# Optimization experiments

Hardware: AMD Instinct MI355X
Metric: run time of the kernel (lower is better)

## Reference

```python
import jax, jax.numpy as jnp
import numpy as np

B = 512
NV = 6890   # SMPL vertices
NJ = 24     # SMPL joints
NB = 10     # shape betas
NP = 207    # pose blend coeffs = 23*9
# canonical SMPL kinematic tree: parent of joints 1..23
PARENT = np.array([0, 0, 0, 1, 2, 3, 4, 5, 6, 7, 8, 9, 9, 9, 12, 13, 14, 16, 17, 18, 19, 20, 21], dtype=np.int64)


def quat2mat(quat):
    # quat: [N,4] (w,x,y,z) -> [N,3,3]
    q = quat / jnp.linalg.norm(quat, axis=1, keepdims=True)
    w, x, y, z = q[:, 0], q[:, 1], q[:, 2], q[:, 3]
    w2, x2, y2, z2 = w * w, x * x, y * y, z * z
    wx, wy, wz = w * x, w * y, w * z
    xy, xz, yz = x * y, x * z, y * z
    rot = jnp.stack([
        w2 + x2 - y2 - z2, 2 * xy - 2 * wz, 2 * wy + 2 * xz,
        2 * wz + 2 * xy, w2 - x2 + y2 - z2, 2 * yz - 2 * wx,
        2 * xz - 2 * wy, 2 * wx + 2 * yz, w2 - x2 - y2 + z2], axis=1)
    return rot.reshape(-1, 3, 3)


def rodrigues(theta):
    # theta: [N,3] axis-angle -> [N,3,3]
    angle = jnp.linalg.norm(theta + 1e-8, axis=1, keepdims=True)
    normalized = theta / angle
    half = angle * 0.5
    quat = jnp.concatenate([jnp.cos(half), jnp.sin(half) * normalized], axis=1)
    return quat2mat(quat)


def setup_inputs() -> dict:
    key = jax.random.key(0)
    ks = jax.random.split(key, 8)
    pose = jax.random.normal(ks[0], (B, NJ * 3), dtype=jnp.float32) * 0.2
    beta = jax.random.normal(ks[1], (B, NB), dtype=jnp.float32)
    v_template = jax.random.normal(ks[2], (NV, 3), dtype=jnp.float32)
    shapedirs = jax.random.normal(ks[3], (NV, 3, NB), dtype=jnp.float32) * 0.01
    posedirs = jax.random.normal(ks[4], (NV, 3, NP), dtype=jnp.float32) * 0.01
    Jr = jax.random.uniform(ks[5], (NJ, NV), dtype=jnp.float32)
    J_regressor = Jr / jnp.sum(Jr, axis=1, keepdims=True)
    W = jax.random.uniform(ks[6], (NV, NJ), dtype=jnp.float32)
    weights = W / jnp.sum(W, axis=1, keepdims=True)
    return {"pose": pose, "beta": beta, "v_template": v_template,
            "shapedirs": shapedirs, "posedirs": posedirs,
            "J_regressor": J_regressor, "weights": weights,
            "parent": PARENT}


def reference(pose, beta, v_template, shapedirs, posedirs, J_regressor, weights, parent):
    dt = pose.dtype
    bsz = pose.shape[0]
    # shape blend: v_shaped [B,V,3]
    v_shaped = jnp.einsum('vdk,bk->bvd', shapedirs, beta) + v_template[None]
    J = jnp.einsum('jv,bvd->bjd', J_regressor, v_shaped)  # [B,24,3]
    # per-joint rotations from axis-angle
    R = rodrigues(pose.reshape(-1, 3)).reshape(bsz, NJ, 3, 3)
    # pose blend
    I3 = jnp.eye(3, dtype=dt)
    lrotmin = (R[:, 1:] - I3).reshape(bsz, NP)
    v_posed = v_shaped + jnp.einsum('vdp,bp->bvd', posedirs, lrotmin)
    # relative joint locations
    J_rel = jnp.concatenate([J[:, :1], J[:, 1:] - J[:, parent]], axis=1)
    # local 4x4 transforms G_local [B,24,4,4]
    bottom = jnp.broadcast_to(jnp.array([0., 0., 0., 1.], dtype=dt).reshape(1, 1, 1, 4), (bsz, NJ, 1, 4))
    G_local = jnp.concatenate([jnp.concatenate([R, J_rel[..., None]], axis=-1), bottom], axis=2)
    # forward kinematics along the tree (24 fixed steps)
    Gs = [G_local[:, 0]]
    for i in range(1, NJ):
        Gs.append(jnp.matmul(Gs[int(parent[i - 1])], G_local[:, i]))
    G = jnp.stack(Gs, axis=1)  # [B,24,4,4]
    # subtract rest-pose joint contribution from translation column
    J_h = jnp.concatenate([J, jnp.zeros((bsz, NJ, 1), dtype=dt)], axis=-1)  # [B,24,4]
    t_corr = jnp.einsum('bjmn,bjn->bjm', G, J_h)
    G = G.at[..., 3].add(-t_corr)
    # linear blend skinning
    T = jnp.einsum('vj,bjmn->bvmn', weights, G)  # [B,V,4,4]
    v_h = jnp.concatenate([v_posed, jnp.ones((bsz, NV, 1), dtype=dt)], axis=-1)
    v = jnp.einsum('bvmn,bvn->bvm', T, v_h)[..., :3]  # [B,V,3]
    return v
```

## Files before the change

kernel.cpp:

```cpp
#include <hip/hip_runtime.h>
#include <hip/hip_bf16.h>
#include <math.h>

#define NVERT 6890
#define NJN   24
#define NBETA 10
#define NPOSE 207
#define NBATCH 512
#define KDIM  224
#define NCOL  20670
#define NPAD  20736

typedef __attribute__((ext_vector_type(8))) short bh8;
typedef __attribute__((ext_vector_type(4))) float f4;

__device__ const int c_parent[23] = {0,0,0,1,2,3,4,5,6,7,8,9,9,9,12,13,14,16,17,18,19,20,21};


__global__ void k_prep(const float* __restrict__ pd, const float* __restrict__ sh,
                       const float* __restrict__ wts,
                       __hip_bfloat16* __restrict__ Bt, float* __restrict__ wT) {
    const int btTotal = NPAD * KDIM;
    const int wtTotal = NJN * NVERT;
    const int total = btTotal + wtTotal;
    for (int idx = blockIdx.x * blockDim.x + threadIdx.x; idx < total;
         idx += gridDim.x * blockDim.x) {
        if (idx < btTotal) {
            int col = idx / KDIM;
            int k = idx - col * KDIM;
            float val = 0.0f;
            if (col < NCOL) {
                int v = col / 3, d = col - v * 3;
                if (k < NPOSE)      val = pd[v * 621 + d * 207 + k];
                else if (k < 217)   val = sh[v * 30 + d * 10 + (k - 207)];
            }
            Bt[idx] = __float2bfloat16(val);
        } else {
            int r = idx - btTotal;
            int j = r / NVERT, v = r - j * NVERT;
            wT[j * 6912 + v] = wts[v * NJN + j];
        }
    }
}

__global__ void k_jreg(const float* __restrict__ Jr, const float* __restrict__ vt,
                       const float* __restrict__ sh, float* __restrict__ jb) {
    const int jd = blockIdx.x;
    const int j = jd / 3, d = jd % 3;
    float acc[11];
#pragma unroll
    for (int k = 0; k < 11; k++) acc[k] = 0.0f;
    for (int v = threadIdx.x; v < NVERT; v += 256) {
        float r = Jr[j * NVERT + v];
        acc[0] += r * vt[v * 3 + d];
        const float* sp = sh + v * 30 + d * 10;
#pragma unroll
        for (int k = 0; k < 10; k++) acc[1 + k] += r * sp[k];
    }
#pragma unroll
    for (int k = 0; k < 11; k++) {
#pragma unroll
        for (int off = 32; off > 0; off >>= 1)
            acc[k] += __shfl_down(acc[k], off);
    }
    __shared__ float red[4][11];
    const int lane = threadIdx.x & 63, wid = threadIdx.x >> 6;
    if (lane == 0) {
#pragma unroll
        for (int k = 0; k < 11; k++) red[wid][k] = acc[k];
    }
    __syncthreads();
    if (threadIdx.x == 0) {
#pragma unroll
        for (int k = 0; k < 11; k++) {
            float s = red[0][k] + red[1][k] + red[2][k] + red[3][k];
            if (k == 0) jb[jd] = s;
            else jb[72 + jd * 10 + (k - 1)] = s;
        }
    }
}

__global__ void k_pose(const float* __restrict__ pose, const float* __restrict__ beta,
                       const float* __restrict__ jb, __hip_bfloat16* __restrict__ A,
                       float* __restrict__ g3) {
    const int b = blockIdx.x, t = threadIdx.x;
    __shared__ float sR[24][9], sJ[24][3], sGl[24][12], sG[24][12];
    if (t < 24) {
        const float* th = pose + b * 72 + t * 3;
        float tx = th[0], ty = th[1], tz = th[2];
        float ax = tx + 1e-8f, ay = ty + 1e-8f, az = tz + 1e-8f;
        float ang = sqrtf(ax * ax + ay * ay + az * az);
        float inv = 1.0f / ang;
        float nx = tx * inv, ny = ty * inv, nz = tz * inv;
        float sw, cw;
        sincosf(0.5f * ang, &sw, &cw);
        float qw = cw, qx = sw * nx, qy = sw * ny, qz = sw * nz;
        float qn = 1.0f / sqrtf(qw * qw + qx * qx + qy * qy + qz * qz);
        qw *= qn; qx *= qn; qy *= qn; qz *= qn;
        float w2 = qw * qw, x2 = qx * qx, y2 = qy * qy, z2 = qz * qz;
        float wx = qw * qx, wy = qw * qy, wz = qw * qz;
        float xy = qx * qy, xz = qx * qz, yz = qy * qz;
        float R[9];
        R[0] = w2 + x2 - y2 - z2; R[1] = 2.f * (xy - wz); R[2] = 2.f * (wy + xz);
        R[3] = 2.f * (wz + xy);   R[4] = w2 - x2 + y2 - z2; R[5] = 2.f * (yz - wx);
        R[6] = 2.f * (xz - wy);   R[7] = 2.f * (wx + yz);   R[8] = w2 - x2 - y2 + z2;
#pragma unroll
        for (int k = 0; k < 9; k++) sR[t][k] = R[k];
        if (t >= 1) {
            __hip_bfloat16* ap = A + b * KDIM + (t - 1) * 9;
#pragma unroll
            for (int k = 0; k < 9; k++)
                ap[k] = __float2bfloat16(R[k] - ((k == 0 || k == 4 || k == 8) ? 1.f : 0.f));
        }
    }
    if (t < NBETA) A[b * KDIM + 207 + t] = __float2bfloat16(beta[b * NBETA + t]);
    if (t < 7)     A[b * KDIM + 217 + t] = __float2bfloat16(0.0f);
    if (t < 72) {
        const int j = t / 3;
        float Jv = jb[t];
        const float* c = jb + 72 + t * 10;
        const float* be = beta + b * NBETA;
#pragma unroll
        for (int k = 0; k < 10; k++) Jv += c[k] * be[k];
        sJ[j][t - j * 3] = Jv;
    }
    __syncthreads();
    if (t < 24) {
#pragma unroll
        for (int r = 0; r < 3; r++) {
            sGl[t][r * 4 + 0] = sR[t][r * 3 + 0];
            sGl[t][r * 4 + 1] = sR[t][r * 3 + 1];
            sGl[t][r * 4 + 2] = sR[t][r * 3 + 2];
            float jr = sJ[t][r];
            if (t > 0) jr -= sJ[c_parent[t - 1]][r];
            sGl[t][r * 4 + 3] = jr;
        }
    }
    __syncthreads();
    if (t < 12) sG[0][t] = sGl[0][t];
    __syncthreads();
    for (int i = 1; i < 24; i++) {
        if (t < 12) {
            const int m = t >> 2, n = t & 3;
            const int p = c_parent[i - 1];
            float val = sG[p][m * 4 + 0] * sGl[i][0 + n]
                      + sG[p][m * 4 + 1] * sGl[i][4 + n]
                      + sG[p][m * 4 + 2] * sGl[i][8 + n];
            if (n == 3) val += sG[p][m * 4 + 3];
            sG[i][t] = val;
        }
        __syncthreads();
    }
    if (t < 24) {
        float jx = sJ[t][0], jy = sJ[t][1], jz = sJ[t][2];
        float* gp = g3 + b * 288 + t * 12;
#pragma unroll
        for (int m = 0; m < 3; m++) {
            float g0 = sG[t][m * 4 + 0], g1 = sG[t][m * 4 + 1];
            float g2 = sG[t][m * 4 + 2], g3v = sG[t][m * 4 + 3];
            float tc = g0 * jx + g1 * jy + g2 * jz;
            gp[m * 4 + 0] = g0; gp[m * 4 + 1] = g1;
            gp[m * 4 + 2] = g2; gp[m * 4 + 3] = g3v - tc;
        }
    }
}

__global__ __launch_bounds__(256) void k_gemm(const __hip_bfloat16* __restrict__ A,
                                              const __hip_bfloat16* __restrict__ Bt,
                                              const float* __restrict__ vt,
                                              float* __restrict__ out) {
    const int lane = threadIdx.x & 63;
    const int wv = threadIdx.x >> 6;
    const int m0 = blockIdx.y * 32;
    const int n0 = blockIdx.x * 256 + wv * 64;
    const int l15 = lane & 15, lg = lane >> 4;

    const short* Ap = (const short*)A + (m0 + l15) * KDIM + lg * 8;
    const short* Bp = (const short*)Bt + (size_t)(n0 + l15) * KDIM + lg * 8;

    f4 acc[2][4];
#pragma unroll
    for (int mt = 0; mt < 2; mt++)
#pragma unroll
        for (int nr = 0; nr < 4; nr++) acc[mt][nr] = (f4){0.f, 0.f, 0.f, 0.f};

#pragma unroll
    for (int kk = 0; kk < 7; kk++) {
        bh8 a0 = *(const bh8*)(Ap + kk * 32);
        bh8 a1 = *(const bh8*)(Ap + 16 * KDIM + kk * 32);
#pragma unroll
        for (int nr = 0; nr < 4; nr++) {
            bh8 b = *(const bh8*)(Bp + (size_t)nr * 16 * KDIM + kk * 32);
            acc[0][nr] = __builtin_amdgcn_mfma_f32_16x16x32_bf16(a0, b, acc[0][nr], 0, 0, 0);
            acc[1][nr] = __builtin_amdgcn_mfma_f32_16x16x32_bf16(a1, b, acc[1][nr], 0, 0, 0);
        }
    }

#pragma unroll
    for (int mt = 0; mt < 2; mt++) {
#pragma unroll
        for (int nr = 0; nr < 4; nr++) {
            int col = n0 + nr * 16 + l15;
            if (col < NCOL) {
                float tv = vt[col];
                int rowb = m0 + mt * 16 + lg * 4;
#pragma unroll
                for (int r = 0; r < 4; r++)
                    out[(size_t)(rowb + r) * NCOL + col] = acc[mt][nr][r] + tv;
            }
        }
    }
}

__global__ __launch_bounds__(256) void k_lbs(const float* __restrict__ g3,
                                             const float* __restrict__ wT,
                                             float* __restrict__ out) {
    __shared__ float sG3[16 * 292];
    const int b0 = blockIdx.x * 16;
    const int v0 = blockIdx.y * 128;
    const int tid = threadIdx.x;
    for (int idx = tid; idx < 16 * 288; idx += 256) {
        int bb = idx / 288, c = idx - bb * 288;
        sG3[bb * 292 + c] = g3[(b0 + bb) * 288 + c];
    }
    __syncthreads();

    const int bg = tid & 7;
    const int vg = tid >> 3;
    int vs[4]; bool vok[4];
#pragma unroll
    for (int s = 0; s < 4; s++) {
        int v = v0 + vg + 32 * s;
        vok[s] = (v < NVERT);
        vs[s] = vok[s] ? v : (NVERT - 1);
    }

    float a[2][4][3];
#pragma unroll
    for (int i = 0; i < 2; i++)
#pragma unroll
        for (int s = 0; s < 4; s++) {
            const float* ap = out + ((size_t)(b0 + bg * 2 + i) * NVERT + vs[s]) * 3;
            a[i][s][0] = ap[0]; a[i][s][1] = ap[1]; a[i][s][2] = ap[2];
        }

#pragma unroll
    for (int i = 0; i < 2; i++) {
        const int bl = bg * 2 + i;
        const float* gb = &sG3[bl * 292];
        float T[4][12];
#pragma unroll
        for (int s = 0; s < 4; s++)
#pragma unroll
            for (int c = 0; c < 12; c++) T[s][c] = 0.0f;
        for (int j = 0; j < 24; j++) {
            float4 g0 = *(const float4*)(gb + j * 12);
            float4 g1 = *(const float4*)(gb + j * 12 + 4);
            float4 g2 = *(const float4*)(gb + j * 12 + 8);
            const float* wrow = wT + j * 6912;
#pragma unroll
            for (int s = 0; s < 4; s++) {
                float wv = wrow[vs[s]];
                T[s][0] += wv * g0.x; T[s][1] += wv * g0.y;
                T[s][2] += wv * g0.z; T[s][3] += wv * g0.w;
                T[s][4] += wv * g1.x; T[s][5] += wv * g1.y;
                T[s][6] += wv * g1.z; T[s][7] += wv * g1.w;
                T[s][8] += wv * g2.x; T[s][9] += wv * g2.y;
                T[s][10] += wv * g2.z; T[s][11] += wv * g2.w;
            }
        }
#pragma unroll
        for (int s = 0; s < 4; s++) {
            float x = a[i][s][0], y = a[i][s][1], z = a[i][s][2];
            float o0 = T[s][0] * x + T[s][1] * y + T[s][2] * z + T[s][3];
            float o1 = T[s][4] * x + T[s][5] * y + T[s][6] * z + T[s][7];
            float o2 = T[s][8] * x + T[s][9] * y + T[s][10] * z + T[s][11];
            if (vok[s]) {
                float* op = out + ((size_t)(b0 + bl) * NVERT + (v0 + vg + 32 * s)) * 3;
                op[0] = o0; op[1] = o1; op[2] = o2;
            }
        }
    }
}

extern "C" void kernel_launch(void* const* d_in, const int* in_sizes, int n_in,
                              void* d_out, int out_size, void* d_ws, size_t ws_size,
                              hipStream_t stream) {
    const float* pose = (const float*)d_in[0];
    const float* beta = (const float*)d_in[1];
    const float* vtm  = (const float*)d_in[2];
    const float* sh   = (const float*)d_in[3];
    const float* pd   = (const float*)d_in[4];
    const float* Jr   = (const float*)d_in[5];
    const float* wts  = (const float*)d_in[6];
    float* out = (float*)d_out;

    __hip_bfloat16* Bt = (__hip_bfloat16*)d_ws;
    __hip_bfloat16* A  = Bt + (size_t)NPAD * KDIM;
    float* g3 = (float*)(A + NBATCH * KDIM);
    float* jb = g3 + NBATCH * 288;
    float* wT = jb + 792;

    k_prep<<<2048, 256, 0, stream>>>(pd, sh, wts, Bt, wT);
    k_jreg<<<72, 256, 0, stream>>>(Jr, vtm, sh, jb);
    k_pose<<<NBATCH, 128, 0, stream>>>(pose, beta, jb, A, g3);
    k_gemm<<<dim3(81, 16), 256, 0, stream>>>(A, Bt, vtm, out);
    k_lbs<<<dim3(32, 54), 256, 0, stream>>>(g3, wT, out);
}
```

Before: 199.2 us.

## Compute skinning transforms with bf16 MFMA instead of scalar FMA loops

The linear blend skinning step now forms the per-vertex 12x24 blended transform through a single 16x16x32 bf16 MFMA per batch and vertex tile. Joint transforms and skinning weights are packed into padded bf16 layouts in the pose and prep kernels, replacing the fp32 shared-memory scalar FMA loop. This cuts ALU work in the skinning kernel but stores transforms and weights in bf16, which lowers precision, including for the translation terms. Output reads and writes also become one scattered component per lane in a per-batch loop.

```diff
diff --git a/kernel.cpp b/kernel.cpp
--- a/kernel.cpp
+++ b/kernel.cpp
@@ -10,6 +10,7 @@
 #define KDIM  224
 #define NCOL  20670
 #define NPAD  20736
+#define VPAD  6912
 
 typedef __attribute__((ext_vector_type(8))) short bh8;
 typedef __attribute__((ext_vector_type(4))) float f4;
@@ -19,10 +20,10 @@
 
 __global__ void k_prep(const float* __restrict__ pd, const float* __restrict__ sh,
                        const float* __restrict__ wts,
-                       __hip_bfloat16* __restrict__ Bt, float* __restrict__ wT) {
+                       __hip_bfloat16* __restrict__ Bt, __hip_bfloat16* __restrict__ Wb) {
     const int btTotal = NPAD * KDIM;
-    const int wtTotal = NJN * NVERT;
-    const int total = btTotal + wtTotal;
+    const int wbTotal = VPAD * 32;
+    const int total = btTotal + wbTotal;
     for (int idx = blockIdx.x * blockDim.x + threadIdx.x; idx < total;
          idx += gridDim.x * blockDim.x) {
         if (idx < btTotal) {
@@ -37,8 +38,9 @@
             Bt[idx] = __float2bfloat16(val);
         } else {
             int r = idx - btTotal;
-            int j = r / NVERT, v = r - j * NVERT;
-            wT[j * 6912 + v] = wts[v * NJN + j];
+            int v = r >> 5, j = r & 31;
+            float val = (v < NVERT && j < NJN) ? wts[v * NJN + j] : 0.0f;
+            Wb[r] = __float2bfloat16(val);
         }
     }
 }
@@ -82,9 +84,9 @@
 
 __global__ void k_pose(const float* __restrict__ pose, const float* __restrict__ beta,
                        const float* __restrict__ jb, __hip_bfloat16* __restrict__ A,
-                       float* __restrict__ g3) {
+                       __hip_bfloat16* __restrict__ Gb) {
     const int b = blockIdx.x, t = threadIdx.x;
-    __shared__ float sR[24][9], sJ[24][3], sGl[24][12], sG[24][12];
+    __shared__ float sR[24][9], sJ[24][3], sGl[24][12], sG[24][12], sT[12][32];
     if (t < 24) {
         const float* th = pose + b * 72 + t * 3;
         float tx = th[0], ty = th[1], tz = th[2];
@@ -153,14 +155,22 @@
     }
     if (t < 24) {
         float jx = sJ[t][0], jy = sJ[t][1], jz = sJ[t][2];
-        float* gp = g3 + b * 288 + t * 12;
 #pragma unroll
         for (int m = 0; m < 3; m++) {
             float g0 = sG[t][m * 4 + 0], g1 = sG[t][m * 4 + 1];
             float g2 = sG[t][m * 4 + 2], g3v = sG[t][m * 4 + 3];
             float tc = g0 * jx + g1 * jy + g2 * jz;
-            gp[m * 4 + 0] = g0; gp[m * 4 + 1] = g1;
-            gp[m * 4 + 2] = g2; gp[m * 4 + 3] = g3v - tc;
+            sT[m * 4 + 0][t] = g0; sT[m * 4 + 1][t] = g1;
+            sT[m * 4 + 2][t] = g2; sT[m * 4 + 3][t] = g3v - tc;
+        }
+    }
+    __syncthreads();
+    if (t < 16) {
+        __hip_bfloat16* gbp = Gb + b * 512 + t * 32;
+#pragma unroll
+        for (int j = 0; j < 32; j++) {
+            float v = (t < 12 && j < 24) ? sT[t][j] : 0.0f;
+            gbp[j] = __float2bfloat16(v);
         }
     }
 }
@@ -212,74 +222,30 @@
     }
 }
 
-__global__ __launch_bounds__(256) void k_lbs(const float* __restrict__ g3,
-                                             const float* __restrict__ wT,
+__global__ __launch_bounds__(256) void k_lbs(const __hip_bfloat16* __restrict__ Gb,
+                                             const __hip_bfloat16* __restrict__ Wb,
                                              float* __restrict__ out) {
-    __shared__ float sG3[16 * 292];
-    const int b0 = blockIdx.x * 16;
-    const int v0 = blockIdx.y * 128;
-    const int tid = threadIdx.x;
-    for (int idx = tid; idx < 16 * 288; idx += 256) {
-        int bb = idx / 288, c = idx - bb * 288;
-        sG3[bb * 292 + c] = g3[(b0 + bb) * 288 + c];
-    }
-    __syncthreads();
-
-    const int bg = tid & 7;
-    const int vg = tid >> 3;
-    int vs[4]; bool vok[4];
-#pragma unroll
-    for (int s = 0; s < 4; s++) {
-        int v = v0 + vg + 32 * s;
-        vok[s] = (v < NVERT);
-        vs[s] = vok[s] ? v : (NVERT - 1);
-    }
-
-    float a[2][4][3];
-#pragma unroll
-    for (int i = 0; i < 2; i++)
-#pragma unroll
-        for (int s = 0; s < 4; s++) {
-            const float* ap = out + ((size_t)(b0 + bg * 2 + i) * NVERT + vs[s]) * 3;
-            a[i][s][0] = ap[0]; a[i][s][1] = ap[1]; a[i][s][2] = ap[2];
-        }
-
-#pragma unroll
-    for (int i = 0; i < 2; i++) {
-        const int bl = bg * 2 + i;
-        const float* gb = &sG3[bl * 292];
-        float T[4][12];
-#pragma unroll
-        for (int s = 0; s < 4; s++)
-#pragma unroll
-            for (int c = 0; c < 12; c++) T[s][c] = 0.0f;
-        for (int j = 0; j < 24; j++) {
-            float4 g0 = *(const float4*)(gb + j * 12);
-            float4 g1 = *(const float4*)(gb + j * 12 + 4);
-            float4 g2 = *(const float4*)(gb + j * 12 + 8);
-            const float* wrow = wT + j * 6912;
-#pragma unroll
-            for (int s = 0; s < 4; s++) {
-                float wv = wrow[vs[s]];
-                T[s][0] += wv * g0.x; T[s][1] += wv * g0.y;
-                T[s][2] += wv * g0.z; T[s][3] += wv * g0.w;
-                T[s][4] += wv * g1.x; T[s][5] += wv * g1.y;
-                T[s][6] += wv * g1.z; T[s][7] += wv * g1.w;
-                T[s][8] += wv * g2.x; T[s][9] += wv * g2.y;
-                T[s][10] += wv * g2.z; T[s][11] += wv * g2.w;
-            }
-        }
-#pragma unroll
-        for (int s = 0; s < 4; s++) {
-            float x = a[i][s][0], y = a[i][s][1], z = a[i][s][2];
-            float o0 = T[s][0] * x + T[s][1] * y + T[s][2] * z + T[s][3];
-            float o1 = T[s][4] * x + T[s][5] * y + T[s][6] * z + T[s][7];
-            float o2 = T[s][8] * x + T[s][9] * y + T[s][10] * z + T[s][11];
-            if (vok[s]) {
-                float* op = out + ((size_t)(b0 + bl) * NVERT + (v0 + vg + 32 * s)) * 3;
-                op[0] = o0; op[1] = o1; op[2] = o2;
-            }
-        }
+    const int w = threadIdx.x >> 6, lane = threadIdx.x & 63;
+    const int l15 = lane & 15, lg = lane >> 4;
+    const int v = blockIdx.x * 64 + w * 16 + l15;
+    const int b0 = blockIdx.y * 64;
+    const bool vreal = (v < NVERT);
+    const int vc = vreal ? v : (NVERT - 1);
+    const bool doio = (lg < 3);
+
+    bh8 wf = *(const bh8*)((const short*)Wb + v * 32 + lg * 8);
+
+    for (int b = b0; b < b0 + 64; b++) {
+        bh8 gf = *(const bh8*)((const short*)Gb + b * 512 + l15 * 32 + lg * 8);
+        f4 T = __builtin_amdgcn_mfma_f32_16x16x32_bf16(gf, wf, (f4){0.f, 0.f, 0.f, 0.f}, 0, 0, 0);
+        float x = 0.f, y = 0.f, z = 0.f;
+        if (doio) {
+            const float* ap = out + ((size_t)b * NVERT + vc) * 3;
+            x = ap[0]; y = ap[1]; z = ap[2];
+        }
+        float val = T[0] * x + T[1] * y + T[2] * z + T[3];
+        if (doio && vreal)
+            out[((size_t)b * NVERT + v) * 3 + lg] = val;
     }
 }
 
@@ -297,13 +263,13 @@
 
     __hip_bfloat16* Bt = (__hip_bfloat16*)d_ws;
     __hip_bfloat16* A  = Bt + (size_t)NPAD * KDIM;
-    float* g3 = (float*)(A + NBATCH * KDIM);
-    float* jb = g3 + NBATCH * 288;
-    float* wT = jb + 792;
-
-    k_prep<<<2048, 256, 0, stream>>>(pd, sh, wts, Bt, wT);
+    __hip_bfloat16* Gb = A + NBATCH * KDIM;
+    __hip_bfloat16* Wb = Gb + NBATCH * 512;
+    float* jb = (float*)(Wb + VPAD * 32);
+
+    k_prep<<<2048, 256, 0, stream>>>(pd, sh, wts, Bt, Wb);
     k_jreg<<<72, 256, 0, stream>>>(Jr, vtm, sh, jb);
-    k_pose<<<NBATCH, 128, 0, stream>>>(pose, beta, jb, A, g3);
+    k_pose<<<NBATCH, 128, 0, stream>>>(pose, beta, jb, A, Gb);
     k_gemm<<<dim3(81, 16), 256, 0, stream>>>(A, Bt, vtm, out);
-    k_lbs<<<dim3(32, 54), 256, 0, stream>>>(g3, wT, out);
-}
+    k_lbs<<<dim3(108, 8), 256, 0, stream>>>(Gb, Wb, out);
+}
```

Result: faster. 191.1 us (-4.1%).
